# Performance work log

Measured on AMD Instinct MI355X. Metric: run time of the kernel, lower is better.

## Reference

```python
import jax, jax.numpy as jnp
import numpy as np

N_NODES = 100000
N_EDGES = 1600000
N_GRAPHS = 100
DIMS = [128, 128, 118, 103, 5]  # in_feats, h, h-10, h-25, num_classes


def setup_inputs() -> dict:
    key = jax.random.key(0)
    ks = jax.random.split(key, 16)
    inp = {
        "in_feat": jax.random.normal(ks[0], (N_NODES, DIMS[0]), dtype=jnp.float32),
        "src": jax.random.randint(ks[1], (N_EDGES,), 0, N_NODES, dtype=jnp.int32),
        "dst": jax.random.randint(ks[2], (N_EDGES,), 0, N_NODES, dtype=jnp.int32),
        "graph_ids": (jnp.arange(N_NODES, dtype=jnp.int32) // (N_NODES // N_GRAPHS)),
    }
    # SAGEConv params: fc_self (no bias), fc_neigh (no bias), shared bias
    for l in range(4):
        din, dout = DIMS[l], DIMS[l + 1]
        inp[f"ws{l+1}"] = jax.random.normal(ks[3 + 3 * l], (din, dout), dtype=jnp.float32) * 0.05
        inp[f"wn{l+1}"] = jax.random.normal(ks[4 + 3 * l], (din, dout), dtype=jnp.float32) * 0.05
        inp[f"b{l+1}"] = jnp.zeros((dout,), dtype=jnp.float32)
    return inp


def reference(in_feat, src, dst, graph_ids,
              ws1, wn1, b1, ws2, wn2, b2, ws3, wn3, b3, ws4, wn4, b4):
    N = in_feat.shape[0]
    # in-degree per dst node, clamped to 1 (DGL: degs.clamp(min=1))
    deg = jnp.clip(jax.ops.segment_sum(jnp.ones((src.shape[0],), in_feat.dtype), dst,
                                       num_segments=N), 1.0, None)

    def sage(h, ws, wn, b):
        # mean-aggregate neighbor features: gather over src, scatter-add to dst
        agg = jax.ops.segment_sum(h[src], dst, num_segments=N) / deg[:, None]
        return h @ ws + agg @ wn + b

    h = jax.nn.relu(sage(in_feat, ws1, wn1, b1))
    h = jax.nn.relu(sage(h, ws2, wn2, b2))
    h = jax.nn.relu(sage(h, ws3, wn3, b3))
    h = sage(h, ws4, wn4, b4)

    # dgl.mean_nodes: per-graph mean pooling over nodes
    ones = jnp.ones((N,), h.dtype)
    cnt = jax.ops.segment_sum(ones, graph_ids, num_segments=N_GRAPHS)
    pooled = jax.ops.segment_sum(h, graph_ids, num_segments=N_GRAPHS) / cnt[:, None]
    return pooled
```

## Files before the change

### kernel.cpp

```cpp
#include <hip/hip_runtime.h>
#include <cstdint>
#include <cstddef>

typedef unsigned int uint32;
typedef unsigned short ushort16;
typedef __attribute__((ext_vector_type(8))) short short8;
typedef __attribute__((ext_vector_type(4))) float floatx4;

__device__ __forceinline__ ushort16 f2bf(float f) {
    uint32 u = __builtin_bit_cast(uint32, f);
    uint32 r = (u + 0x7fffu + ((u >> 16) & 1u)) >> 16;
    return (ushort16)r;
}
__device__ __forceinline__ float bf2f(ushort16 h) {
    uint32 u = ((uint32)h) << 16;
    return __builtin_bit_cast(float, u);
}

#define PBS 4096

__global__ __launch_bounds__(256) void bucket_hist_kernel(
    const int* __restrict__ dst, int* __restrict__ bcnt, int E, int NBUCK) {
    __shared__ int l[512];
    int t = threadIdx.x;
    for (int b = t; b < NBUCK; b += 256) l[b] = 0;
    __syncthreads();
    int e0 = blockIdx.x * PBS;
    int e1 = e0 + PBS; if (e1 > E) e1 = E;
    for (int j = e0 + t; j < e1; j += 256)
        atomicAdd(&l[dst[j] >> 8], 1);
    __syncthreads();
    for (int b = t; b < NBUCK; b += 256) {
        int c = l[b];
        if (c) atomicAdd(&bcnt[b], c);
    }
}

__global__ __launch_bounds__(256) void bucket_scan_kernel(
    const int* __restrict__ bcnt, int* __restrict__ bucketOff,
    int* __restrict__ cursorA, int NBUCK, int E) {
    __shared__ int a[512], b[512];
    int t = threadIdx.x;
    a[t] = (t < NBUCK) ? bcnt[t] : 0;
    a[t + 256] = (t + 256 < NBUCK) ? bcnt[t + 256] : 0;
    __syncthreads();
    int* cur = a; int* nxt = b;
    for (int o = 1; o < 512; o <<= 1) {
#pragma unroll
        for (int i = t; i < 512; i += 256)
            nxt[i] = cur[i] + ((i >= o) ? cur[i - o] : 0);
        __syncthreads();
        int* tmp = cur; cur = nxt; nxt = tmp;
    }
#pragma unroll
    for (int i = t; i < 512; i += 256) {
        if (i <= NBUCK) {
            int off = (i == 0) ? 0 : cur[i - 1];
            bucketOff[i] = off;
            if (i < NBUCK) cursorA[i] = off;
        }
    }
    if (t == 0) bucketOff[NBUCK] = E;
}

__global__ __launch_bounds__(256) void bucket_partition_kernel(
    const int* __restrict__ src, const int* __restrict__ dst,
    int* __restrict__ cursorA, uint32* __restrict__ ebuf, int E, int NBUCK) {
    __shared__ int lbase[512];
    int tid = threadIdx.x;
    for (int b = tid; b < NBUCK; b += 256) lbase[b] = 0;
    __syncthreads();
    int e0 = blockIdx.x * PBS;
    int e1 = e0 + PBS; if (e1 > E) e1 = E;
    for (int j = e0 + tid; j < e1; j += 256)
        atomicAdd(&lbase[dst[j] >> 8], 1);
    __syncthreads();
    for (int b = tid; b < NBUCK; b += 256) {
        int c = lbase[b];
        lbase[b] = c ? atomicAdd(&cursorA[b], c) : 0;
    }
    __syncthreads();
    for (int j = e0 + tid; j < e1; j += 256) {
        int d = dst[j];
        int p = atomicAdd(&lbase[d >> 8], 1);
        ebuf[p] = ((uint32)src[j] << 8) | (uint32)(d & 255);
    }
}

__global__ __launch_bounds__(256) void bucket_build_kernel(
    const uint32* __restrict__ ebuf, const int* __restrict__ bucketOff,
    int* __restrict__ row_ptr, float* __restrict__ degf,
    int* __restrict__ csr, int N, int E) {
    __shared__ int ldeg[256];
    __shared__ int lscan[256];
    __shared__ int lcur[256];
    int b = blockIdx.x, t = threadIdx.x;
    int n0 = b << 8;
    int s = bucketOff[b], e = bucketOff[b + 1];
    ldeg[t] = 0;
    __syncthreads();
    for (int j = s + t; j < e; j += 256)
        atomicAdd(&ldeg[ebuf[j] & 255u], 1);
    __syncthreads();
    int v = ldeg[t];
    lscan[t] = v;
    __syncthreads();
    for (int off = 1; off < 256; off <<= 1) {
        int x = (t >= off) ? lscan[t - off] : 0;
        __syncthreads();
        lscan[t] += x;
        __syncthreads();
    }
    int excl = lscan[t] - v;
    int node = n0 + t;
    if (node < N) {
        row_ptr[node] = s + excl;
        degf[node] = (float)(v > 0 ? v : 1);
    }
    lcur[t] = s + excl;
    __syncthreads();
    for (int j = s + t; j < e; j += 256) {
        uint32 en = ebuf[j];
        int p = atomicAdd(&lcur[en & 255u], 1);
        csr[p] = (int)(en >> 8);
    }
    if (b == 0 && t == 0) row_ptr[N] = E;
}

__global__ void conv_bf16_kernel(const float* __restrict__ x, ushort16* __restrict__ y, int n8) {
    int i = blockIdx.x * blockDim.x + threadIdx.x;
    if (i >= n8) return;
    const float4 a = *(const float4*)(x + (size_t)i * 8);
    const float4 b = *(const float4*)(x + (size_t)i * 8 + 4);
    uint4 o;
    o.x = (uint32)f2bf(a.x) | ((uint32)f2bf(a.y) << 16);
    o.y = (uint32)f2bf(a.z) | ((uint32)f2bf(a.w) << 16);
    o.z = (uint32)f2bf(b.x) | ((uint32)f2bf(b.y) << 16);
    o.w = (uint32)f2bf(b.z) | ((uint32)f2bf(b.w) << 16);
    *(uint4*)(y + (size_t)i * 8) = o;
}

__global__ void prep_w_all_kernel(
    const float* __restrict__ W0s, const float* __restrict__ W0n,
    const float* __restrict__ W1s, const float* __restrict__ W1n,
    const float* __restrict__ W2s, const float* __restrict__ W2n,
    ushort16* __restrict__ Whi, ushort16* __restrict__ Wlo) {
    int mat = blockIdx.x >> 6;
    int idx = (blockIdx.x & 63) * 256 + threadIdx.x;
    const float* Wt[6] = {W0s, W0n, W1s, W1n, W2s, W2n};
    const int Kt[6] = {128, 128, 128, 128, 118, 118};
    const int Mt[6] = {128, 128, 118, 118, 103, 103};
    int n = idx >> 7, k = idx & 127;
    int K = Kt[mat], M = Mt[mat];
    float w = (k < K && n < M) ? Wt[mat][(size_t)k * M + n] : 0.f;
    ushort16 h = f2bf(w);
    float lo = w - bf2f(h);
    Whi[(size_t)mat * 16384 + idx] = h;
    Wlo[(size_t)mat * 16384 + idx] = f2bf(lo);
}

template<int UNROLL>
__global__ __launch_bounds__(256) void aggregate_pre_kernel(
    const ushort16* __restrict__ h,
    const int* __restrict__ row_ptr, const int* __restrict__ csr,
    const float* __restrict__ degf, ushort16* __restrict__ aggH, int N) {
    int wid = threadIdx.x >> 6;
    int lane = threadIdx.x & 63;
    int node = blockIdx.x * 4 + wid;
    if (node >= N) return;
    int s = row_ptr[node], e = row_ptr[node + 1];
    int c = lane & 15;
    int eo = lane >> 4;
    float aLo[4] = {}, aHi[4] = {};
    int j = s + eo;
    for (; j + (UNROLL - 1) * 4 < e; j += UNROLL * 4) {
        uint4 v[UNROLL];
#pragma unroll
        for (int u = 0; u < UNROLL; ++u) {
            int src_n = csr[j + u * 4];
            v[u] = *(const uint4*)(h + ((size_t)src_n << 7) + (c << 3));
        }
#pragma unroll
        for (int u = 0; u < UNROLL; ++u) {
            uint32 w[4] = {v[u].x, v[u].y, v[u].z, v[u].w};
#pragma unroll
            for (int p = 0; p < 4; ++p) {
                aLo[p] += __builtin_bit_cast(float, w[p] << 16);
                aHi[p] += __builtin_bit_cast(float, w[p] & 0xffff0000u);
            }
        }
    }
    for (; j < e; j += 4) {
        int src_n = csr[j];
        uint4 v = *(const uint4*)(h + ((size_t)src_n << 7) + (c << 3));
        uint32 w[4] = {v.x, v.y, v.z, v.w};
#pragma unroll
        for (int p = 0; p < 4; ++p) {
            aLo[p] += __builtin_bit_cast(float, w[p] << 16);
            aHi[p] += __builtin_bit_cast(float, w[p] & 0xffff0000u);
        }
    }
#pragma unroll
    for (int m = 16; m < 64; m <<= 1) {
#pragma unroll
        for (int p = 0; p < 4; ++p) {
            aLo[p] += __shfl_xor(aLo[p], m, 64);
            aHi[p] += __shfl_xor(aHi[p], m, 64);
        }
    }
    if (lane < 16) {
        float inv = 1.f / degf[node];
        uint4 ov;
        ov.x = (uint32)f2bf(aLo[0] * inv) | ((uint32)f2bf(aHi[0] * inv) << 16);
        ov.y = (uint32)f2bf(aLo[1] * inv) | ((uint32)f2bf(aHi[1] * inv) << 16);
        ov.z = (uint32)f2bf(aLo[2] * inv) | ((uint32)f2bf(aHi[2] * inv) << 16);
        ov.w = (uint32)f2bf(aLo[3] * inv) | ((uint32)f2bf(aHi[3] * inv) << 16);
        *(uint4*)(aggH + ((size_t)node << 7) + (c << 3)) = ov;
    }
}

__global__ __launch_bounds__(256) void mfma_fused_kernel(
    const ushort16* __restrict__ A, const ushort16* __restrict__ G,
    const ushort16* __restrict__ Whi, const ushort16* __restrict__ Wlo,
    const float* __restrict__ bias,
    ushort16* __restrict__ Out, int N, int M) {
    const int tid = threadIdx.x;
    const int wave = tid >> 6;
    const int lane = tid & 63;
    const int quad = lane >> 4;
    const int m16 = lane & 15;

    const int ct = blockIdx.y * 4 + wave;
    const int colt = ct * 16 + m16;

    short8 bsh[4], bsl[4], bnh[4], bnl[4];
    {
        const size_t wo = (size_t)colt * 128 + quad * 8;
#pragma unroll
        for (int ks = 0; ks < 4; ++ks) {
            bsh[ks] = *(const short8*)(Whi + wo + ks * 32);
            bsl[ks] = *(const short8*)(Wlo + wo + ks * 32);
            bnh[ks] = *(const short8*)(Whi + 16384 + wo + ks * 32);
            bnl[ks] = *(const short8*)(Wlo + 16384 + wo + ks * 32);
        }
    }
    const bool inc = (colt < M);
    const float bv = inc ? bias[colt] : 0.f;

    const int r0 = blockIdx.x * 128;
#pragma unroll
    for (int it = 0; it < 4; ++it) {
        const int rbase = r0 + it * 32;
        int ra0 = rbase + m16;       if (ra0 >= N) ra0 = N - 1;
        int ra1 = rbase + 16 + m16;  if (ra1 >= N) ra1 = N - 1;
        const ushort16* A0 = A + ((size_t)ra0 << 7) + quad * 8;
        const ushort16* G0 = G + ((size_t)ra0 << 7) + quad * 8;
        const ushort16* A1 = A + ((size_t)ra1 << 7) + quad * 8;
        const ushort16* G1 = G + ((size_t)ra1 << 7) + quad * 8;
        short8 a0[4], g0[4], a1[4], g1[4];
#pragma unroll
        for (int ks = 0; ks < 4; ++ks) {
            a0[ks] = *(const short8*)(A0 + ks * 32);
            g0[ks] = *(const short8*)(G0 + ks * 32);
            a1[ks] = *(const short8*)(A1 + ks * 32);
            g1[ks] = *(const short8*)(G1 + ks * 32);
        }
        floatx4 acc0 = {}, acc1 = {};
#pragma unroll
        for (int ks = 0; ks < 4; ++ks) {
            acc0 = __builtin_amdgcn_mfma_f32_16x16x32_bf16(a0[ks], bsh[ks], acc0, 0, 0, 0);
            acc1 = __builtin_amdgcn_mfma_f32_16x16x32_bf16(a1[ks], bsh[ks], acc1, 0, 0, 0);
            acc0 = __builtin_amdgcn_mfma_f32_16x16x32_bf16(g0[ks], bnh[ks], acc0, 0, 0, 0);
            acc1 = __builtin_amdgcn_mfma_f32_16x16x32_bf16(g1[ks], bnh[ks], acc1, 0, 0, 0);
            acc0 = __builtin_amdgcn_mfma_f32_16x16x32_bf16(a0[ks], bsl[ks], acc0, 0, 0, 0);
            acc1 = __builtin_amdgcn_mfma_f32_16x16x32_bf16(a1[ks], bsl[ks], acc1, 0, 0, 0);
            acc0 = __builtin_amdgcn_mfma_f32_16x16x32_bf16(g0[ks], bnl[ks], acc0, 0, 0, 0);
            acc1 = __builtin_amdgcn_mfma_f32_16x16x32_bf16(g1[ks], bnl[ks], acc1, 0, 0, 0);
        }
#pragma unroll
        for (int r = 0; r < 4; ++r) {
            int row0 = rbase + quad * 4 + r;
            if (row0 < N) {
                float v = inc ? fmaxf(acc0[r] + bv, 0.f) : 0.f;
                Out[(size_t)row0 * 128 + colt] = f2bf(v);
            }
            int row1 = rbase + 16 + quad * 4 + r;
            if (row1 < N) {
                float v = inc ? fmaxf(acc1[r] + bv, 0.f) : 0.f;
                Out[(size_t)row1 * 128 + colt] = f2bf(v);
            }
        }
    }
}

__global__ __launch_bounds__(256) void gemm4_kernel(
    const ushort16* __restrict__ A, const float* __restrict__ ws,
    const float* __restrict__ wn, const float* __restrict__ b4,
    float* __restrict__ Cs, float* __restrict__ Cn, int N, int K, int M) {
    __shared__ float Wsh[520], Wnh[520];
    int tid = threadIdx.x;
    for (int i = tid; i < K * M; i += 256) { Wsh[i] = ws[i]; Wnh[i] = wn[i]; }
    __syncthreads();
    int node = blockIdx.x * 256 + tid;
    if (node >= N) return;
    const ushort16* row = A + ((size_t)node << 7);
    float s[5] = {}, n[5] = {};
    for (int c8 = 0; c8 * 8 < K; ++c8) {
        uint4 v = *(const uint4*)(row + c8 * 8);
        uint32 w[4] = {v.x, v.y, v.z, v.w};
#pragma unroll
        for (int j = 0; j < 8; ++j) {
            int k = c8 * 8 + j;
            if (k < K) {
                float a = (j & 1) ? __builtin_bit_cast(float, w[j >> 1] & 0xffff0000u)
                                  : __builtin_bit_cast(float, w[j >> 1] << 16);
#pragma unroll
                for (int m = 0; m < 5; ++m) {
                    s[m] += a * Wsh[k * 5 + m];
                    n[m] += a * Wnh[k * 5 + m];
                }
            }
        }
    }
    size_t o = (size_t)node * 8;
#pragma unroll
    for (int m = 0; m < 5; ++m) {
        Cs[o + m] = s[m] + b4[m];
        Cn[o + m] = n[m];
    }
#pragma unroll
    for (int m = 5; m < 8; ++m) { Cs[o + m] = 0.f; Cn[o + m] = 0.f; }
}

template<int CPW, int UNROLL, int SLOG>
__global__ __launch_bounds__(256) void aggregate_fp32_kernel(
    const float* __restrict__ hs, const float* __restrict__ hn,
    const int* __restrict__ row_ptr, const int* __restrict__ csr,
    const float* __restrict__ degf, float* __restrict__ out, int N) {
    constexpr int EPI = 64 / CPW;
    int wid = threadIdx.x >> 6;
    int lane = threadIdx.x & 63;
    int node = blockIdx.x * 4 + wid;
    if (node >= N) return;
    int s = row_ptr[node], e = row_ptr[node + 1];
    int c = lane & (CPW - 1);
    int eo = lane / CPW;
    float4 acc = make_float4(0.f, 0.f, 0.f, 0.f);
    int j = s + eo;
    for (; j + (UNROLL - 1) * EPI < e; j += UNROLL * EPI) {
        float4 v[UNROLL];
#pragma unroll
        for (int u = 0; u < UNROLL; ++u) {
            int src_n = csr[j + u * EPI];
            v[u] = *(const float4*)(hn + ((size_t)src_n << SLOG) + (c << 2));
        }
#pragma unroll
        for (int u = 0; u < UNROLL; ++u) {
            acc.x += v[u].x; acc.y += v[u].y; acc.z += v[u].z; acc.w += v[u].w;
        }
    }
    for (; j < e; j += EPI) {
        int src_n = csr[j];
        float4 v = *(const float4*)(hn + ((size_t)src_n << SLOG) + (c << 2));
        acc.x += v.x; acc.y += v.y; acc.z += v.z; acc.w += v.w;
    }
#pragma unroll
    for (int m = CPW; m < 64; m <<= 1) {
        acc.x += __shfl_xor(acc.x, m, 64);
        acc.y += __shfl_xor(acc.y, m, 64);
        acc.z += __shfl_xor(acc.z, m, 64);
        acc.w += __shfl_xor(acc.w, m, 64);
    }
    if (lane < CPW) {
        float d = 1.f / degf[node];
        size_t o = ((size_t)node << SLOG) + (lane << 2);
        float4 hv = *(const float4*)(hs + o);
        float4 r;
        r.x = hv.x + acc.x * d;
        r.y = hv.y + acc.y * d;
        r.z = hv.z + acc.z * d;
        r.w = hv.w + acc.w * d;
        *(float4*)(out + o) = r;
    }
}

__global__ __launch_bounds__(256) void pool_kernel(
    const float* __restrict__ h, float* __restrict__ out, int npg) {
    __shared__ float sh[4][5];
    int g = blockIdx.x;
    int t = threadIdx.x;
    float acc[5] = {0.f, 0.f, 0.f, 0.f, 0.f};
    int base = g * npg;
    for (int i = t; i < npg; i += 256) {
        const float* r = h + ((size_t)(base + i) << 3);
#pragma unroll
        for (int f = 0; f < 5; ++f) acc[f] += r[f];
    }
#pragma unroll
    for (int off = 32; off > 0; off >>= 1) {
#pragma unroll
        for (int f = 0; f < 5; ++f) acc[f] += __shfl_down(acc[f], off, 64);
    }
    int wid = t >> 6, lane = t & 63;
    if (lane == 0) {
#pragma unroll
        for (int f = 0; f < 5; ++f) sh[wid][f] = acc[f];
    }
    __syncthreads();
    if (t == 0) {
        float inv = 1.f / (float)npg;
#pragma unroll
        for (int f = 0; f < 5; ++f)
            out[g * 5 + f] = (sh[0][f] + sh[1][f] + sh[2][f] + sh[3][f]) * inv;
    }
}

extern "C" void kernel_launch(void* const* d_in, const int* in_sizes, int n_in,
                              void* d_out, int out_size, void* d_ws, size_t ws_size,
                              hipStream_t stream) {
    const float* in_feat = (const float*)d_in[0];
    const int* src = (const int*)d_in[1];
    const int* dst = (const int*)d_in[2];
    const int DIMS[5] = {128, 128, 118, 103, 5};
    const int N = in_sizes[0] / 128;
    const int E = in_sizes[1];
    const int G = out_size / 5;
    const int NBUCK = (N + 255) >> 8;

    char* base = (char*)d_ws;
    size_t off = 0;
    auto carve = [&](size_t bytes) -> void* {
        off = (off + 255) & ~(size_t)255;
        void* p = base + off;
        off += bytes;
        return p;
    };
    int* bcnt = (int*)carve((size_t)NBUCK * 4);
    int* bucketOff = (int*)carve((size_t)(NBUCK + 1) * 4);
    int* cursorA = (int*)carve((size_t)NBUCK * 4);
    int* row_ptr = (int*)carve((size_t)(N + 1) * 4);
    float* degf = (float*)carve((size_t)N * 4);
    uint32* ebuf = (uint32*)carve((size_t)E * 4);
    int* csr = (int*)carve((size_t)E * 4);
    ushort16* buf0 = (ushort16*)carve((size_t)(N + 256) * 128 * 2);
    ushort16* buf1 = (ushort16*)carve((size_t)(N + 256) * 128 * 2);
    ushort16* aggH = (ushort16*)carve((size_t)(N + 256) * 128 * 2);
    ushort16* Whi = (ushort16*)carve((size_t)6 * 16384 * 2);
    ushort16* Wlo = (ushort16*)carve((size_t)6 * 16384 * 2);
    float* Cs4 = (float*)carve((size_t)N * 8 * 4);
    float* Cn4 = (float*)carve((size_t)N * 8 * 4);
    float* out4 = (float*)carve((size_t)N * 8 * 4);
    (void)n_in; (void)ws_size;

    hipMemsetAsync(bcnt, 0, (size_t)NBUCK * 4, stream);
    bucket_hist_kernel<<<(E + PBS - 1) / PBS, 256, 0, stream>>>(dst, bcnt, E, NBUCK);
    bucket_scan_kernel<<<1, 256, 0, stream>>>(bcnt, bucketOff, cursorA, NBUCK, E);
    bucket_partition_kernel<<<(E + PBS - 1) / PBS, 256, 0, stream>>>(
        src, dst, cursorA, ebuf, E, NBUCK);
    bucket_build_kernel<<<NBUCK, 256, 0, stream>>>(
        ebuf, bucketOff, row_ptr, degf, csr, N, E);

    int n8 = N * 16;
    conv_bf16_kernel<<<(n8 + 255) / 256, 256, 0, stream>>>(in_feat, buf0, n8);
    prep_w_all_kernel<<<6 * 64, 256, 0, stream>>>(
        (const float*)d_in[4], (const float*)d_in[5],
        (const float*)d_in[7], (const float*)d_in[8],
        (const float*)d_in[10], (const float*)d_in[11],
        Whi, Wlo);

    ushort16* hb[4] = {buf0, buf1, buf0, buf1};
    dim3 ggrid((N + 127) / 128, 2);
    for (int l = 0; l < 3; ++l) {
        int M = DIMS[l + 1];
        const float* b = (const float*)d_in[6 + 3 * l];
        aggregate_pre_kernel<4><<<(N + 3) / 4, 256, 0, stream>>>(
            hb[l], row_ptr, csr, degf, aggH, N);
        mfma_fused_kernel<<<ggrid, 256, 0, stream>>>(
            hb[l], aggH, Whi + (size_t)l * 2 * 16384, Wlo + (size_t)l * 2 * 16384,
            b, hb[l + 1], N, M);
    }

    gemm4_kernel<<<(N + 255) / 256, 256, 0, stream>>>(
        hb[3], (const float*)d_in[13], (const float*)d_in[14], (const float*)d_in[15],
        Cs4, Cn4, N, DIMS[3], DIMS[4]);
    aggregate_fp32_kernel<2, 1, 3><<<(N + 3) / 4, 256, 0, stream>>>(
        Cs4, Cn4, row_ptr, csr, degf, out4, N);
    pool_kernel<<<G, 256, 0, stream>>>(out4, (float*)d_out, N / G);
}
```

Measured before the change: 605.8 us.

## Double-buffer row tiles in fused MFMA SAGE kernel and skip empty column waves

Restructures the fused self/neighbour MFMA kernel to walk 256 rows per block in 16-row steps. The A and G tiles for the next step are prefetched into a second register buffer while the current step's MFMAs run, so global load latency overlaps with compute. It also adds an early return for waves whose 16-column tile lies entirely past M, sets launch_bounds occupancy to 2, and pins the weight fragments in registers with an empty asm. In exchange it uses more registers per thread, launches fewer blocks, and leaves padding columns past M unwritten when a whole wave is skipped.

```diff
diff --git a/kernel.cpp b/kernel.cpp
--- a/kernel.cpp
+++ b/kernel.cpp
@@ -219,7 +219,22 @@
     }
 }
 
-__global__ __launch_bounds__(256) void mfma_fused_kernel(
+__device__ __forceinline__ void load_tile16(
+    short8 a[4], short8 g[4],
+    const ushort16* __restrict__ A, const ushort16* __restrict__ G,
+    int rbase, int N, int m16, int quad) {
+    int ra = rbase + m16;
+    if (ra >= N) ra = N - 1;
+    const ushort16* Ar = A + ((size_t)ra << 7) + quad * 8;
+    const ushort16* Gr = G + ((size_t)ra << 7) + quad * 8;
+#pragma unroll
+    for (int ks = 0; ks < 4; ++ks) {
+        a[ks] = *(const short8*)(Ar + ks * 32);
+        g[ks] = *(const short8*)(Gr + ks * 32);
+    }
+}
+
+__global__ __launch_bounds__(256, 2) void mfma_fused_kernel(
     const ushort16* __restrict__ A, const ushort16* __restrict__ G,
     const ushort16* __restrict__ Whi, const ushort16* __restrict__ Wlo,
     const float* __restrict__ bias,
@@ -231,6 +246,7 @@
     const int m16 = lane & 15;
 
     const int ct = blockIdx.y * 4 + wave;
+    if (ct * 16 >= M) return;
     const int colt = ct * 16 + m16;
 
     short8 bsh[4], bsl[4], bnh[4], bnl[4];
@@ -244,50 +260,42 @@
             bnl[ks] = *(const short8*)(Wlo + 16384 + wo + ks * 32);
         }
     }
+#pragma unroll
+    for (int ks = 0; ks < 4; ++ks) {
+        asm volatile("" : "+v"(bsh[ks]), "+v"(bsl[ks]), "+v"(bnh[ks]), "+v"(bnl[ks]));
+    }
+
     const bool inc = (colt < M);
     const float bv = inc ? bias[colt] : 0.f;
-
-    const int r0 = blockIdx.x * 128;
-#pragma unroll
-    for (int it = 0; it < 4; ++it) {
-        const int rbase = r0 + it * 32;
-        int ra0 = rbase + m16;       if (ra0 >= N) ra0 = N - 1;
-        int ra1 = rbase + 16 + m16;  if (ra1 >= N) ra1 = N - 1;
-        const ushort16* A0 = A + ((size_t)ra0 << 7) + quad * 8;
-        const ushort16* G0 = G + ((size_t)ra0 << 7) + quad * 8;
-        const ushort16* A1 = A + ((size_t)ra1 << 7) + quad * 8;
-        const ushort16* G1 = G + ((size_t)ra1 << 7) + quad * 8;
-        short8 a0[4], g0[4], a1[4], g1[4];
+    const int r0 = blockIdx.x * 256;
+
+    short8 aA[4], gA[4], aB[4], gB[4];
+    load_tile16(aA, gA, A, G, r0, N, m16, quad);
+
+#pragma unroll
+    for (int t = 0; t < 16; ++t) {
+        short8* ca = (t & 1) ? aB : aA;
+        short8* cg = (t & 1) ? gB : gA;
+        short8* na = (t & 1) ? aA : aB;
+        short8* ng = (t & 1) ? gA : gB;
+        if (t < 15)
+            load_tile16(na, ng, A, G, r0 + (t + 1) * 16, N, m16, quad);
+
+        floatx4 acc = {};
 #pragma unroll
         for (int ks = 0; ks < 4; ++ks) {
-            a0[ks] = *(const short8*)(A0 + ks * 32);
-            g0[ks] = *(const short8*)(G0 + ks * 32);
-            a1[ks] = *(const short8*)(A1 + ks * 32);
-            g1[ks] = *(const short8*)(G1 + ks * 32);
-        }
-        floatx4 acc0 = {}, acc1 = {};
-#pragma unroll
-        for (int ks = 0; ks < 4; ++ks) {
-            acc0 = __builtin_amdgcn_mfma_f32_16x16x32_bf16(a0[ks], bsh[ks], acc0, 0, 0, 0);
-            acc1 = __builtin_amdgcn_mfma_f32_16x16x32_bf16(a1[ks], bsh[ks], acc1, 0, 0, 0);
-            acc0 = __builtin_amdgcn_mfma_f32_16x16x32_bf16(g0[ks], bnh[ks], acc0, 0, 0, 0);
-            acc1 = __builtin_amdgcn_mfma_f32_16x16x32_bf16(g1[ks], bnh[ks], acc1, 0, 0, 0);
-            acc0 = __builtin_amdgcn_mfma_f32_16x16x32_bf16(a0[ks], bsl[ks], acc0, 0, 0, 0);
-            acc1 = __builtin_amdgcn_mfma_f32_16x16x32_bf16(a1[ks], bsl[ks], acc1, 0, 0, 0);
-            acc0 = __builtin_amdgcn_mfma_f32_16x16x32_bf16(g0[ks], bnl[ks], acc0, 0, 0, 0);
-            acc1 = __builtin_amdgcn_mfma_f32_16x16x32_bf16(g1[ks], bnl[ks], acc1, 0, 0, 0);
-        }
+            acc = __builtin_amdgcn_mfma_f32_16x16x32_bf16(ca[ks], bsh[ks], acc, 0, 0, 0);
+            acc = __builtin_amdgcn_mfma_f32_16x16x32_bf16(cg[ks], bnh[ks], acc, 0, 0, 0);
+            acc = __builtin_amdgcn_mfma_f32_16x16x32_bf16(ca[ks], bsl[ks], acc, 0, 0, 0);
+            acc = __builtin_amdgcn_mfma_f32_16x16x32_bf16(cg[ks], bnl[ks], acc, 0, 0, 0);
+        }
+        const int rbase = r0 + t * 16 + quad * 4;
 #pragma unroll
         for (int r = 0; r < 4; ++r) {
-            int row0 = rbase + quad * 4 + r;
-            if (row0 < N) {
-                float v = inc ? fmaxf(acc0[r] + bv, 0.f) : 0.f;
-                Out[(size_t)row0 * 128 + colt] = f2bf(v);
-            }
-            int row1 = rbase + 16 + quad * 4 + r;
-            if (row1 < N) {
-                float v = inc ? fmaxf(acc1[r] + bv, 0.f) : 0.f;
-                Out[(size_t)row1 * 128 + colt] = f2bf(v);
+            int row = rbase + r;
+            if (row < N) {
+                float v = inc ? fmaxf(acc[r] + bv, 0.f) : 0.f;
+                Out[(size_t)row * 128 + colt] = f2bf(v);
             }
         }
     }
@@ -469,7 +477,7 @@
         Whi, Wlo);
 
     ushort16* hb[4] = {buf0, buf1, buf0, buf1};
-    dim3 ggrid((N + 127) / 128, 2);
+    dim3 ggrid((N + 255) / 256, 2);
     for (int l = 0; l < 3; ++l) {
         int M = DIMS[l + 1];
         const float* b = (const float*)d_in[6 + 3 * l];
```

Measured after the change: 610.8 us. About the same (+0.8%).
